# Kernel optimization log

Measured on AMD Instinct MI355X. Metric: run time of the kernel, lower is better.

Reference implementation:

```python
import jax, jax.numpy as jnp
import numpy as np

B, M, FIN, OUT, K = 64, 512, 128, 128, 2
SLOPE = 0.01  # F.leaky_relu default negative_slope


def setup_inputs() -> dict:
    key = jax.random.key(0)
    k0, k1, k2, k3 = jax.random.split(key, 4)
    x = jax.random.normal(k0, (B, M, FIN), jnp.float32)
    La = jax.random.normal(k1, (B, M, M), jnp.float32)
    weight = jax.random.normal(k2, (FIN * K, OUT), jnp.float32) * np.sqrt(2.0 / (FIN * K + OUT))
    bias = jnp.zeros((OUT,), jnp.float32)
    M_L = jax.random.normal(k3, (FIN, FIN), jnp.float32) * np.sqrt(2.0 / FIN)
    return {"x": x, "La": La, "weight": weight, "bias": bias, "M_L": M_L}


def _leaky(v):
    return jnp.where(v >= 0, v, SLOPE * v)


def _per_mol(xm, Lm, weight, bias, M_L):
    # xm: [M, FIN], Lm: [M, M]
    # compute_laplacian: pairwise Euclidean distances of x @ M_L via gram trick
    xw = xm @ M_L                                   # [M, FIN]
    sq = jnp.sum(xw * xw, axis=-1)                  # [M]
    d2 = sq[:, None] + sq[None, :] - 2.0 * (xw @ xw.T)
    dist = jnp.sqrt(jnp.maximum(d2, 1e-12))         # safe sqrt (diag is 0)
    W = jnp.exp(-dist)                              # [M, M]
    d = W.sum(axis=1) + 1e-7
    dis = 1.0 / jnp.sqrt(d)
    L = jnp.eye(M, dtype=xm.dtype) - dis[:, None] * W * dis[None, :]
    # clip_by_average_norm(clip_norm=1)
    avg_norm = jnp.linalg.norm(L) / (M * M)
    factor = jnp.minimum(1.0 / (avg_norm + 1e-6), 1.0)
    res_L = _leaky(L * factor)
    L_all = res_L + Lm
    # Chebyshev recursion (K terms)
    xs = [xm]
    if K > 1:
        xs.append(L_all @ xm)
    for _ in range(2, K):
        xs.append(2.0 * (L_all @ xs[-1]) - xs[-2])
    xk = jnp.stack(xs, axis=0)                      # [K, M, FIN]
    xk = jnp.transpose(xk, (1, 2, 0)).reshape(M, K * FIN)  # matches permute(1,2,0).view
    out = _leaky(xk @ weight + bias)                # activation 'relu' maps to leaky_relu
    return out, res_L, W


def reference(x, La, weight, bias, M_L):
    out, L_upd, W_upd = jax.vmap(lambda xm, Lm: _per_mol(xm, Lm, weight, bias, M_L))(x, La)
    return out, L_upd, W_upd
```

## Files before the change

kernel.cpp:

```cpp
#include <hip/hip_runtime.h>


#define BB 64
#define MM 512
#define FINC 128
#define OUTC 128

typedef short bf16x8 __attribute__((ext_vector_type(8)));
typedef float f32x4 __attribute__((ext_vector_type(4)));

__device__ __forceinline__ float leaky_(float v) { return v >= 0.0f ? v : 0.01f * v; }
__device__ __forceinline__ unsigned short f2bf(float f) {
    unsigned int u = __float_as_uint(f);
    return (unsigned short)((u + 0x7FFF + ((u >> 16) & 1)) >> 16);
}

__global__ __launch_bounds__(256) void k_xw(const float* __restrict__ x,
                                            const float* __restrict__ ml,
                                            unsigned short* __restrict__ xwb,
                                            float* __restrict__ sq,
                                            unsigned short* __restrict__ xTb) {
    const int b = blockIdx.y, i0 = blockIdx.x * 64;
    const int tid = threadIdx.x, ty4 = (tid >> 4) * 4, tx4 = (tid & 15) * 4;
    __shared__ float a_t[64][129];
    __shared__ float b_t[64][129];
    __shared__ float red[64][17];

    const float* xb = x + ((size_t)b * MM + i0) * FINC;
#pragma unroll
    for (int q = 0; q < 8; ++q) {
        int idx4 = tid + q * 256;
        int r = idx4 >> 5, k4 = (idx4 & 31) * 4;
        float4 v = *(const float4*)(xb + r * FINC + k4);
        a_t[r][k4 + 0] = v.x; a_t[r][k4 + 1] = v.y;
        a_t[r][k4 + 2] = v.z; a_t[r][k4 + 3] = v.w;
    }

    float acc[4][8];
#pragma unroll
    for (int m = 0; m < 4; ++m)
#pragma unroll
        for (int n = 0; n < 8; ++n) acc[m][n] = 0.0f;

    for (int kc = 0; kc < 2; ++kc) {
        __syncthreads();
#pragma unroll
        for (int q = 0; q < 8; ++q) {
            int idx4 = tid + q * 256;
            int kk = idx4 >> 5, c4 = (idx4 & 31) * 4;
            float4 v = *(const float4*)(ml + (size_t)(kc * 64 + kk) * FINC + c4);
            b_t[kk][c4 + 0] = v.x; b_t[kk][c4 + 1] = v.y;
            b_t[kk][c4 + 2] = v.z; b_t[kk][c4 + 3] = v.w;
        }
        __syncthreads();
#pragma unroll 4
        for (int k = 0; k < 64; ++k) {
            float av[4], bv[8];
#pragma unroll
            for (int m = 0; m < 4; ++m) av[m] = a_t[ty4 + m][kc * 64 + k];
#pragma unroll
            for (int n = 0; n < 4; ++n) { bv[n] = b_t[k][tx4 + n]; bv[4 + n] = b_t[k][64 + tx4 + n]; }
#pragma unroll
            for (int m = 0; m < 4; ++m)
#pragma unroll
                for (int n = 0; n < 8; ++n) acc[m][n] = fmaf(av[m], bv[n], acc[m][n]);
        }
    }

    unsigned short* xwbb = xwb + ((size_t)b * MM + i0) * FINC;
#pragma unroll
    for (int m = 0; m < 4; ++m) {
        ushort4 h0, h1;
        h0.x = f2bf(acc[m][0]); h0.y = f2bf(acc[m][1]); h0.z = f2bf(acc[m][2]); h0.w = f2bf(acc[m][3]);
        h1.x = f2bf(acc[m][4]); h1.y = f2bf(acc[m][5]); h1.z = f2bf(acc[m][6]); h1.w = f2bf(acc[m][7]);
        *(ushort4*)(xwbb + (ty4 + m) * FINC + tx4) = h0;
        *(ushort4*)(xwbb + (ty4 + m) * FINC + 64 + tx4) = h1;
        float p = 0.0f;
#pragma unroll
        for (int n = 0; n < 8; ++n) p = fmaf(acc[m][n], acc[m][n], p);
        red[ty4 + m][tid & 15] = p;
    }
    __syncthreads();
    if (tid < 64) {
        float s = 0.0f;
#pragma unroll
        for (int t = 0; t < 16; ++t) s += red[tid][t];
        sq[b * MM + i0 + tid] = s;
    }
#pragma unroll
    for (int q = 0; q < 16; ++q) {
        int idx = tid + q * 256;
        int c = idx >> 5, j2 = (idx & 31) * 2;
        ushort2 t;
        t.x = f2bf(a_t[j2][c]);
        t.y = f2bf(a_t[j2 + 1][c]);
        *(ushort2*)(xTb + ((size_t)b * FINC + c) * MM + i0 + j2) = t;
    }
}

__global__ __launch_bounds__(256) void k_gram(const unsigned short* __restrict__ xwb,
                                              const float* __restrict__ sq,
                                              float* __restrict__ Wout,
                                              float* __restrict__ dis) {
    const int b = blockIdx.y, i0 = blockIdx.x * 64;
    const int tid = threadIdx.x;
    const int w = tid >> 6, l = tid & 63, lr = l & 15, lg = l >> 4;
    const unsigned short* xb = xwb + (size_t)b * MM * FINC;
    const int ia = i0 + w * 16 + lr;
    const unsigned short* arow = xb + (size_t)ia * FINC + lg * 8;
    bf16x8 a0 = *(const bf16x8*)(arow + 0);
    bf16x8 a1 = *(const bf16x8*)(arow + 32);
    bf16x8 a2 = *(const bf16x8*)(arow + 64);
    bf16x8 a3 = *(const bf16x8*)(arow + 96);

    const int id0 = i0 + w * 16 + lg * 4;
    const float* sqb = sq + b * MM;
    const float si0 = sqb[id0 + 0], si1 = sqb[id0 + 1], si2 = sqb[id0 + 2], si3 = sqb[id0 + 3];
    float rs0 = 0.f, rs1 = 0.f, rs2 = 0.f, rs3 = 0.f;
    float* Wb = Wout + (size_t)b * MM * MM;

#pragma unroll 2
    for (int h = 0; h < 2; ++h) {
        const int j0 = h * 256;
#pragma unroll
        for (int n = 0; n < 16; ++n) {
            const int jc = j0 + n * 16 + lr;
            const unsigned short* jrow = xb + (size_t)jc * FINC + lg * 8;
            bf16x8 b0 = *(const bf16x8*)(jrow + 0);
            bf16x8 b1 = *(const bf16x8*)(jrow + 32);
            bf16x8 b2 = *(const bf16x8*)(jrow + 64);
            bf16x8 b3 = *(const bf16x8*)(jrow + 96);
            f32x4 acc = {0.f, 0.f, 0.f, 0.f};
            acc = __builtin_amdgcn_mfma_f32_16x16x32_bf16(a0, b0, acc, 0, 0, 0);
            acc = __builtin_amdgcn_mfma_f32_16x16x32_bf16(a1, b1, acc, 0, 0, 0);
            acc = __builtin_amdgcn_mfma_f32_16x16x32_bf16(a2, b2, acc, 0, 0, 0);
            acc = __builtin_amdgcn_mfma_f32_16x16x32_bf16(a3, b3, acc, 0, 0, 0);
            const float sj = sqb[jc];
            float d2, wv;
            d2 = si0 + sj - 2.f * acc[0]; if (id0 + 0 == jc) d2 = 0.f;
            wv = __expf(-sqrtf(fmaxf(d2, 1e-12f)));
            Wb[(size_t)(id0 + 0) * MM + jc] = wv; rs0 += wv;
            d2 = si1 + sj - 2.f * acc[1]; if (id0 + 1 == jc) d2 = 0.f;
            wv = __expf(-sqrtf(fmaxf(d2, 1e-12f)));
            Wb[(size_t)(id0 + 1) * MM + jc] = wv; rs1 += wv;
            d2 = si2 + sj - 2.f * acc[2]; if (id0 + 2 == jc) d2 = 0.f;
            wv = __expf(-sqrtf(fmaxf(d2, 1e-12f)));
            Wb[(size_t)(id0 + 2) * MM + jc] = wv; rs2 += wv;
            d2 = si3 + sj - 2.f * acc[3]; if (id0 + 3 == jc) d2 = 0.f;
            wv = __expf(-sqrtf(fmaxf(d2, 1e-12f)));
            Wb[(size_t)(id0 + 3) * MM + jc] = wv; rs3 += wv;
        }
    }
#pragma unroll
    for (int msk = 1; msk < 16; msk <<= 1) {
        rs0 += __shfl_xor(rs0, msk);
        rs1 += __shfl_xor(rs1, msk);
        rs2 += __shfl_xor(rs2, msk);
        rs3 += __shfl_xor(rs3, msk);
    }
    if (lr == 0) {
        dis[b * MM + id0 + 0] = 1.0f / sqrtf(rs0 + 1e-7f);
        dis[b * MM + id0 + 1] = 1.0f / sqrtf(rs1 + 1e-7f);
        dis[b * MM + id0 + 2] = 1.0f / sqrtf(rs2 + 1e-7f);
        dis[b * MM + id0 + 3] = 1.0f / sqrtf(rs3 + 1e-7f);
    }
}

__global__ __launch_bounds__(256) void k_norm(const float* __restrict__ Wout,
                                              const float* __restrict__ dis,
                                              float* __restrict__ norm2) {
    const int b = blockIdx.y;
    const float4* Wb4 = (const float4*)(Wout + (size_t)b * MM * MM);
    const float* disb = dis + b * MM;
    const int base4 = blockIdx.x * 4096;
    float acc = 0.0f;
#pragma unroll 4
    for (int q = 0; q < 16; ++q) {
        int idx4 = base4 + q * 256 + threadIdx.x;
        float4 w = Wb4[idx4];
        int p = idx4 * 4, i = p >> 9, j = p & 511;
        float di = disb[i];
        float4 dj = *(const float4*)(disb + j);
        float l0 = ((i == j + 0) ? 1.0f : 0.0f) - di * w.x * dj.x;
        float l1 = ((i == j + 1) ? 1.0f : 0.0f) - di * w.y * dj.y;
        float l2 = ((i == j + 2) ? 1.0f : 0.0f) - di * w.z * dj.z;
        float l3 = ((i == j + 3) ? 1.0f : 0.0f) - di * w.w * dj.w;
        acc += l0 * l0 + l1 * l1 + l2 * l2 + l3 * l3;
    }
#pragma unroll
    for (int off = 32; off > 0; off >>= 1) acc += __shfl_down(acc, off);
    __shared__ float r[4];
    if ((threadIdx.x & 63) == 0) r[threadIdx.x >> 6] = acc;
    __syncthreads();
    if (threadIdx.x == 0) atomicAdd(&norm2[b], r[0] + r[1] + r[2] + r[3]);
}

__global__ void k_factor(const float* __restrict__ norm2, float* __restrict__ factor) {
    int t = threadIdx.x;
    if (t < BB) {
        float avg = sqrtf(norm2[t]) / (512.0f * 512.0f);
        factor[t] = fminf(1.0f / (avg + 1e-6f), 1.0f);
    }
}

__global__ __launch_bounds__(256) void k_wt(const float* __restrict__ weight,
                                            unsigned short* __restrict__ wTb) {
    int tid = threadIdx.x;
#pragma unroll 4
    for (int q = 0; q < 128; ++q) {
        int idx = tid + q * 256;
        int k = idx >> 7, c = idx & 127;
        wTb[(size_t)c * 256 + k] = f2bf(weight[idx]);
    }
}

__global__ __launch_bounds__(256) void k_lall(const float* __restrict__ Wout,
                                              const float* __restrict__ La,
                                              const unsigned short* __restrict__ xTb,
                                              const float* __restrict__ dis,
                                              const float* __restrict__ factor,
                                              float* __restrict__ resL,
                                              unsigned short* __restrict__ yb) {
    const int b = blockIdx.y, i0 = blockIdx.x * 64;
    const int tid = threadIdx.x;
    const int w = tid >> 6, l = tid & 63, lr = l & 15, lg = l >> 4;
    const int ia = i0 + w * 16 + lr;
    const float fac = factor[b];
    const float* disb = dis + b * MM;
    const float di = disb[ia];
    const float* Wr = Wout + (size_t)b * MM * MM + (size_t)ia * MM;
    const float* Lr = La   + (size_t)b * MM * MM + (size_t)ia * MM;
    float* Rr = resL + (size_t)b * MM * MM + (size_t)ia * MM;
    const unsigned short* xTm = xTb + (size_t)b * FINC * MM;

    f32x4 acc[8];
#pragma unroll
    for (int n = 0; n < 8; ++n) acc[n] = (f32x4){0.f, 0.f, 0.f, 0.f};

    int ko0 = lg * 8;
    float4 wc0 = *(const float4*)(Wr + ko0), wc1 = *(const float4*)(Wr + ko0 + 4);
    float4 lc0 = *(const float4*)(Lr + ko0), lc1 = *(const float4*)(Lr + ko0 + 4);

#pragma unroll
    for (int t = 0; t < 16; ++t) {
        const int koff = t * 32 + lg * 8;
        float4 wn0, wn1, ln0, ln1;
        if (t < 15) {
            const int kn = (t + 1) * 32 + lg * 8;
            wn0 = *(const float4*)(Wr + kn); wn1 = *(const float4*)(Wr + kn + 4);
            ln0 = *(const float4*)(Lr + kn); ln1 = *(const float4*)(Lr + kn + 4);
        }
        float4 dj0 = *(const float4*)(disb + koff);
        float4 dj1 = *(const float4*)(disb + koff + 4);

        const int dd = ia - koff;
        const float* wp0 = &wc0.x; const float* wp1 = &wc1.x;
        const float* lp0 = &lc0.x; const float* lp1 = &lc1.x;
        const float* dp0 = &dj0.x; const float* dp1 = &dj1.x;
        float4 r0, r1; float* rp0 = &r0.x; float* rp1 = &r1.x;
        bf16x8 af;
#pragma unroll
        for (int e = 0; e < 4; ++e) {
            float Lv = ((dd == e) ? 1.0f : 0.0f) - di * wp0[e] * dp0[e];
            float rv = leaky_(Lv * fac);
            rp0[e] = rv;
            af[e] = (short)f2bf(rv + lp0[e]);
        }
#pragma unroll
        for (int e = 0; e < 4; ++e) {
            float Lv = ((dd == e + 4) ? 1.0f : 0.0f) - di * wp1[e] * dp1[e];
            float rv = leaky_(Lv * fac);
            rp1[e] = rv;
            af[e + 4] = (short)f2bf(rv + lp1[e]);
        }
        *(float4*)(Rr + koff) = r0;
        *(float4*)(Rr + koff + 4) = r1;

#pragma unroll
        for (int n = 0; n < 8; ++n) {
            bf16x8 bf = *(const bf16x8*)(xTm + (size_t)(n * 16 + lr) * MM + koff);
            acc[n] = __builtin_amdgcn_mfma_f32_16x16x32_bf16(af, bf, acc[n], 0, 0, 0);
        }
        wc0 = wn0; wc1 = wn1; lc0 = ln0; lc1 = ln1;
    }

    const int id0 = i0 + w * 16 + lg * 4;
    unsigned short* ybb = yb + (size_t)b * MM * FINC;
#pragma unroll
    for (int n = 0; n < 8; ++n) {
        const int col = n * 16 + lr;
#pragma unroll
        for (int rg = 0; rg < 4; ++rg)
            ybb[(size_t)(id0 + rg) * FINC + col] = f2bf(acc[n][rg]);
    }
}

__global__ __launch_bounds__(256) void k_out(const float* __restrict__ x,
                                             const unsigned short* __restrict__ yb,
                                             const unsigned short* __restrict__ wTb,
                                             const float* __restrict__ bias,
                                             float* __restrict__ out) {
    const int b = blockIdx.y, i0 = blockIdx.x * 64;
    const int tid = threadIdx.x;
    const int w = tid >> 6, l = tid & 63, lr = l & 15, lg = l >> 4;
    const int ia = i0 + w * 16 + lr;
    const float* xr = x + ((size_t)b * MM + ia) * FINC;
    const unsigned short* yr = yb + ((size_t)b * MM + ia) * FINC;

    f32x4 acc[8];
#pragma unroll
    for (int n = 0; n < 8; ++n) acc[n] = (f32x4){0.f, 0.f, 0.f, 0.f};

#pragma unroll
    for (int ch = 0; ch < 8; ++ch) {
        const int koff = ch * 32 + lg * 8;
        const int f0 = koff >> 1;
        float4 xv = *(const float4*)(xr + f0);
        ushort4 yv = *(const ushort4*)(yr + f0);
        bf16x8 af;
        af[0] = (short)f2bf(xv.x); af[1] = (short)yv.x;
        af[2] = (short)f2bf(xv.y); af[3] = (short)yv.y;
        af[4] = (short)f2bf(xv.z); af[5] = (short)yv.z;
        af[6] = (short)f2bf(xv.w); af[7] = (short)yv.w;
#pragma unroll
        for (int n = 0; n < 8; ++n) {
            bf16x8 bf = *(const bf16x8*)(wTb + (size_t)(n * 16 + lr) * 256 + koff);
            acc[n] = __builtin_amdgcn_mfma_f32_16x16x32_bf16(af, bf, acc[n], 0, 0, 0);
        }
    }

    const int id0 = i0 + w * 16 + lg * 4;
    float* ob = out + (size_t)b * MM * OUTC;
#pragma unroll
    for (int n = 0; n < 8; ++n) {
        const int col = n * 16 + lr;
        const float bs = bias[col];
#pragma unroll
        for (int rg = 0; rg < 4; ++rg)
            ob[(size_t)(id0 + rg) * OUTC + col] = leaky_(acc[n][rg] + bs);
    }
}

extern "C" void kernel_launch(void* const* d_in, const int* in_sizes, int n_in,
                              void* d_out, int out_size, void* d_ws, size_t ws_size,
                              hipStream_t stream) {
    const float* x      = (const float*)d_in[0];
    const float* La     = (const float*)d_in[1];
    const float* weight = (const float*)d_in[2];
    const float* bias   = (const float*)d_in[3];
    const float* ml     = (const float*)d_in[4];

    float* out0 = (float*)d_out;
    float* out1 = out0 + (size_t)BB * MM * OUTC;
    float* out2 = out1 + (size_t)BB * MM * MM;

    unsigned short* xwb = (unsigned short*)d_ws;
    unsigned short* yb  = xwb;
    unsigned short* xTb = xwb + 4194304;
    float* sq     = (float*)((char*)d_ws + 16777216);
    unsigned short* wTb = (unsigned short*)sq;
    float* dis    = sq + 32768;
    float* norm2  = dis + 32768;
    float* factor = norm2 + 64;

    hipMemsetAsync(norm2, 0, BB * sizeof(float), stream);

    dim3 blk(256);
    k_xw    <<<dim3(8, BB), blk, 0, stream>>>(x, ml, xwb, sq, xTb);
    k_gram  <<<dim3(8, BB), blk, 0, stream>>>(xwb, sq, out2, dis);
    k_norm  <<<dim3(16, BB), blk, 0, stream>>>(out2, dis, norm2);
    k_factor<<<1, 64, 0, stream>>>(norm2, factor);
    k_wt    <<<1, blk, 0, stream>>>(weight, wTb);
    k_lall  <<<dim3(8, BB), blk, 0, stream>>>(out2, La, xTb, dis, factor, out1, yb);
    k_out   <<<dim3(8, BB), blk, 0, stream>>>(x, yb, wTb, bias, out0);
}
```

Measured before the change: 397.2 us.

## Software-prefetch operands in gram, lall and out kernels; fold factor and weight kernels

Restructures the k_gram column loop into 32 tiles that prefetch the next tile's bf16 rows and sq value while the current MFMA and exp work runs. k_lall now uses two-deep register prefetch of W/La rows and batches its B-operand loads ahead of the MFMAs. k_out prefetches the next x/y chunk. The factor computation moves into k_lall and the weight transpose into block (0,0) of k_norm, which removes two small launches. The cost is higher register pressure, which could reduce occupancy.

```diff
diff --git a/kernel.cpp b/kernel.cpp
--- a/kernel.cpp
+++ b/kernel.cpp
@@ -119,37 +119,45 @@
     float rs0 = 0.f, rs1 = 0.f, rs2 = 0.f, rs3 = 0.f;
     float* Wb = Wout + (size_t)b * MM * MM;
 
-#pragma unroll 2
-    for (int h = 0; h < 2; ++h) {
-        const int j0 = h * 256;
-#pragma unroll
-        for (int n = 0; n < 16; ++n) {
-            const int jc = j0 + n * 16 + lr;
-            const unsigned short* jrow = xb + (size_t)jc * FINC + lg * 8;
-            bf16x8 b0 = *(const bf16x8*)(jrow + 0);
-            bf16x8 b1 = *(const bf16x8*)(jrow + 32);
-            bf16x8 b2 = *(const bf16x8*)(jrow + 64);
-            bf16x8 b3 = *(const bf16x8*)(jrow + 96);
-            f32x4 acc = {0.f, 0.f, 0.f, 0.f};
-            acc = __builtin_amdgcn_mfma_f32_16x16x32_bf16(a0, b0, acc, 0, 0, 0);
-            acc = __builtin_amdgcn_mfma_f32_16x16x32_bf16(a1, b1, acc, 0, 0, 0);
-            acc = __builtin_amdgcn_mfma_f32_16x16x32_bf16(a2, b2, acc, 0, 0, 0);
-            acc = __builtin_amdgcn_mfma_f32_16x16x32_bf16(a3, b3, acc, 0, 0, 0);
-            const float sj = sqb[jc];
-            float d2, wv;
-            d2 = si0 + sj - 2.f * acc[0]; if (id0 + 0 == jc) d2 = 0.f;
-            wv = __expf(-sqrtf(fmaxf(d2, 1e-12f)));
-            Wb[(size_t)(id0 + 0) * MM + jc] = wv; rs0 += wv;
-            d2 = si1 + sj - 2.f * acc[1]; if (id0 + 1 == jc) d2 = 0.f;
-            wv = __expf(-sqrtf(fmaxf(d2, 1e-12f)));
-            Wb[(size_t)(id0 + 1) * MM + jc] = wv; rs1 += wv;
-            d2 = si2 + sj - 2.f * acc[2]; if (id0 + 2 == jc) d2 = 0.f;
-            wv = __expf(-sqrtf(fmaxf(d2, 1e-12f)));
-            Wb[(size_t)(id0 + 2) * MM + jc] = wv; rs2 += wv;
-            d2 = si3 + sj - 2.f * acc[3]; if (id0 + 3 == jc) d2 = 0.f;
-            wv = __expf(-sqrtf(fmaxf(d2, 1e-12f)));
-            Wb[(size_t)(id0 + 3) * MM + jc] = wv; rs3 += wv;
-        }
+    const unsigned short* jr0 = xb + (size_t)lr * FINC + lg * 8;
+    bf16x8 c0 = *(const bf16x8*)(jr0 + 0);
+    bf16x8 c1 = *(const bf16x8*)(jr0 + 32);
+    bf16x8 c2 = *(const bf16x8*)(jr0 + 64);
+    bf16x8 c3 = *(const bf16x8*)(jr0 + 96);
+    float sjc = sqb[lr];
+
+#pragma unroll
+    for (int tl = 0; tl < 32; ++tl) {
+        const int nt = (tl < 31) ? tl + 1 : 31;
+        const unsigned short* nr = xb + (size_t)(nt * 16 + lr) * FINC + lg * 8;
+        bf16x8 n0 = *(const bf16x8*)(nr + 0);
+        bf16x8 n1 = *(const bf16x8*)(nr + 32);
+        bf16x8 n2 = *(const bf16x8*)(nr + 64);
+        bf16x8 n3 = *(const bf16x8*)(nr + 96);
+        float sjn = sqb[nt * 16 + lr];
+
+        f32x4 acc = {0.f, 0.f, 0.f, 0.f};
+        acc = __builtin_amdgcn_mfma_f32_16x16x32_bf16(a0, c0, acc, 0, 0, 0);
+        acc = __builtin_amdgcn_mfma_f32_16x16x32_bf16(a1, c1, acc, 0, 0, 0);
+        acc = __builtin_amdgcn_mfma_f32_16x16x32_bf16(a2, c2, acc, 0, 0, 0);
+        acc = __builtin_amdgcn_mfma_f32_16x16x32_bf16(a3, c3, acc, 0, 0, 0);
+
+        const int jc = tl * 16 + lr;
+        float d2, wv;
+        d2 = si0 + sjc - 2.f * acc[0]; if (id0 + 0 == jc) d2 = 0.f;
+        wv = __expf(-sqrtf(fmaxf(d2, 1e-12f)));
+        Wb[(size_t)(id0 + 0) * MM + jc] = wv; rs0 += wv;
+        d2 = si1 + sjc - 2.f * acc[1]; if (id0 + 1 == jc) d2 = 0.f;
+        wv = __expf(-sqrtf(fmaxf(d2, 1e-12f)));
+        Wb[(size_t)(id0 + 1) * MM + jc] = wv; rs1 += wv;
+        d2 = si2 + sjc - 2.f * acc[2]; if (id0 + 2 == jc) d2 = 0.f;
+        wv = __expf(-sqrtf(fmaxf(d2, 1e-12f)));
+        Wb[(size_t)(id0 + 2) * MM + jc] = wv; rs2 += wv;
+        d2 = si3 + sjc - 2.f * acc[3]; if (id0 + 3 == jc) d2 = 0.f;
+        wv = __expf(-sqrtf(fmaxf(d2, 1e-12f)));
+        Wb[(size_t)(id0 + 3) * MM + jc] = wv; rs3 += wv;
+
+        c0 = n0; c1 = n1; c2 = n2; c3 = n3; sjc = sjn;
     }
 #pragma unroll
     for (int msk = 1; msk < 16; msk <<= 1) {
@@ -168,7 +176,9 @@
 
 __global__ __launch_bounds__(256) void k_norm(const float* __restrict__ Wout,
                                               const float* __restrict__ dis,
-                                              float* __restrict__ norm2) {
+                                              float* __restrict__ norm2,
+                                              const float* __restrict__ weight,
+                                              unsigned short* __restrict__ wTb) {
     const int b = blockIdx.y;
     const float4* Wb4 = (const float4*)(Wout + (size_t)b * MM * MM);
     const float* disb = dis + b * MM;
@@ -193,24 +203,15 @@
     if ((threadIdx.x & 63) == 0) r[threadIdx.x >> 6] = acc;
     __syncthreads();
     if (threadIdx.x == 0) atomicAdd(&norm2[b], r[0] + r[1] + r[2] + r[3]);
-}
-
-__global__ void k_factor(const float* __restrict__ norm2, float* __restrict__ factor) {
-    int t = threadIdx.x;
-    if (t < BB) {
-        float avg = sqrtf(norm2[t]) / (512.0f * 512.0f);
-        factor[t] = fminf(1.0f / (avg + 1e-6f), 1.0f);
-    }
-}
-
-__global__ __launch_bounds__(256) void k_wt(const float* __restrict__ weight,
-                                            unsigned short* __restrict__ wTb) {
-    int tid = threadIdx.x;
+
+    if (blockIdx.x == 0 && blockIdx.y == 0) {
+        int tid = threadIdx.x;
 #pragma unroll 4
-    for (int q = 0; q < 128; ++q) {
-        int idx = tid + q * 256;
-        int k = idx >> 7, c = idx & 127;
-        wTb[(size_t)c * 256 + k] = f2bf(weight[idx]);
+        for (int q = 0; q < 128; ++q) {
+            int idx = tid + q * 256;
+            int k = idx >> 7, c = idx & 127;
+            wTb[(size_t)c * 256 + k] = f2bf(weight[idx]);
+        }
     }
 }
 
@@ -218,14 +219,15 @@
                                               const float* __restrict__ La,
                                               const unsigned short* __restrict__ xTb,
                                               const float* __restrict__ dis,
-                                              const float* __restrict__ factor,
+                                              const float* __restrict__ norm2,
                                               float* __restrict__ resL,
                                               unsigned short* __restrict__ yb) {
     const int b = blockIdx.y, i0 = blockIdx.x * 64;
     const int tid = threadIdx.x;
     const int w = tid >> 6, l = tid & 63, lr = l & 15, lg = l >> 4;
     const int ia = i0 + w * 16 + lr;
-    const float fac = factor[b];
+    const float avgn = sqrtf(norm2[b]) / (512.0f * 512.0f);
+    const float fac = fminf(1.0f / (avgn + 1e-6f), 1.0f);
     const float* disb = dis + b * MM;
     const float di = disb[ia];
     const float* Wr = Wout + (size_t)b * MM * MM + (size_t)ia * MM;
@@ -237,52 +239,60 @@
 #pragma unroll
     for (int n = 0; n < 8; ++n) acc[n] = (f32x4){0.f, 0.f, 0.f, 0.f};
 
-    int ko0 = lg * 8;
-    float4 wc0 = *(const float4*)(Wr + ko0), wc1 = *(const float4*)(Wr + ko0 + 4);
-    float4 lc0 = *(const float4*)(Lr + ko0), lc1 = *(const float4*)(Lr + ko0 + 4);
-
-#pragma unroll
-    for (int t = 0; t < 16; ++t) {
-        const int koff = t * 32 + lg * 8;
-        float4 wn0, wn1, ln0, ln1;
-        if (t < 15) {
-            const int kn = (t + 1) * 32 + lg * 8;
-            wn0 = *(const float4*)(Wr + kn); wn1 = *(const float4*)(Wr + kn + 4);
-            ln0 = *(const float4*)(Lr + kn); ln1 = *(const float4*)(Lr + kn + 4);
-        }
-        float4 dj0 = *(const float4*)(disb + koff);
-        float4 dj1 = *(const float4*)(disb + koff + 4);
-
-        const int dd = ia - koff;
-        const float* wp0 = &wc0.x; const float* wp1 = &wc1.x;
-        const float* lp0 = &lc0.x; const float* lp1 = &lc1.x;
-        const float* dp0 = &dj0.x; const float* dp1 = &dj1.x;
-        float4 r0, r1; float* rp0 = &r0.x; float* rp1 = &r1.x;
-        bf16x8 af;
-#pragma unroll
-        for (int e = 0; e < 4; ++e) {
-            float Lv = ((dd == e) ? 1.0f : 0.0f) - di * wp0[e] * dp0[e];
-            float rv = leaky_(Lv * fac);
-            rp0[e] = rv;
-            af[e] = (short)f2bf(rv + lp0[e]);
-        }
-#pragma unroll
-        for (int e = 0; e < 4; ++e) {
-            float Lv = ((dd == e + 4) ? 1.0f : 0.0f) - di * wp1[e] * dp1[e];
-            float rv = leaky_(Lv * fac);
-            rp1[e] = rv;
-            af[e + 4] = (short)f2bf(rv + lp1[e]);
-        }
-        *(float4*)(Rr + koff) = r0;
-        *(float4*)(Rr + koff + 4) = r1;
-
-#pragma unroll
-        for (int n = 0; n < 8; ++n) {
-            bf16x8 bf = *(const bf16x8*)(xTm + (size_t)(n * 16 + lr) * MM + koff);
-            acc[n] = __builtin_amdgcn_mfma_f32_16x16x32_bf16(af, bf, acc[n], 0, 0, 0);
-        }
-        wc0 = wn0; wc1 = wn1; lc0 = ln0; lc1 = ln1;
-    }
+#define LD2(W0, W1, L0, L1, t) { const int kk_ = (t) * 32 + lg * 8; \
+    W0 = *(const float4*)(Wr + kk_); W1 = *(const float4*)(Wr + kk_ + 4); \
+    L0 = *(const float4*)(Lr + kk_); L1 = *(const float4*)(Lr + kk_ + 4); }
+
+#define STEP(CW0, CW1, CL0, CL1, t) { \
+    const int koff = (t) * 32 + lg * 8; \
+    bf16x8 bfr[8]; \
+    _Pragma("unroll") \
+    for (int n = 0; n < 8; ++n) \
+        bfr[n] = *(const bf16x8*)(xTm + (size_t)(n * 16 + lr) * MM + koff); \
+    float4 dj0 = *(const float4*)(disb + koff); \
+    float4 dj1 = *(const float4*)(disb + koff + 4); \
+    const int dd = ia - koff; \
+    const float* wp0 = &CW0.x; const float* wp1 = &CW1.x; \
+    const float* lp0 = &CL0.x; const float* lp1 = &CL1.x; \
+    const float* dp0 = &dj0.x; const float* dp1 = &dj1.x; \
+    float4 r0, r1; float* rp0 = &r0.x; float* rp1 = &r1.x; \
+    bf16x8 af; \
+    _Pragma("unroll") \
+    for (int e = 0; e < 4; ++e) { \
+        float Lv = ((dd == e) ? 1.0f : 0.0f) - di * wp0[e] * dp0[e]; \
+        float rv = leaky_(Lv * fac); \
+        rp0[e] = rv; \
+        af[e] = (short)f2bf(rv + lp0[e]); \
+    } \
+    _Pragma("unroll") \
+    for (int e = 0; e < 4; ++e) { \
+        float Lv = ((dd == e + 4) ? 1.0f : 0.0f) - di * wp1[e] * dp1[e]; \
+        float rv = leaky_(Lv * fac); \
+        rp1[e] = rv; \
+        af[e + 4] = (short)f2bf(rv + lp1[e]); \
+    } \
+    *(float4*)(Rr + koff) = r0; \
+    *(float4*)(Rr + koff + 4) = r1; \
+    _Pragma("unroll") \
+    for (int n = 0; n < 8; ++n) \
+        acc[n] = __builtin_amdgcn_mfma_f32_16x16x32_bf16(af, bfr[n], acc[n], 0, 0, 0); \
+}
+
+    float4 aw0, aw1, al0, al1, bw0, bw1, bl0, bl1, tw0, tw1, tl0, tl1;
+    LD2(aw0, aw1, al0, al1, 0);
+    LD2(bw0, bw1, bl0, bl1, 1);
+#pragma unroll
+    for (int tp = 0; tp < 8; ++tp) {
+        const int t0 = tp * 2, t1 = tp * 2 + 1;
+        if (t0 + 2 < 16) { LD2(tw0, tw1, tl0, tl1, t0 + 2); }
+        STEP(aw0, aw1, al0, al1, t0);
+        if (t0 + 2 < 16) { aw0 = tw0; aw1 = tw1; al0 = tl0; al1 = tl1; }
+        if (t1 + 2 < 16) { LD2(tw0, tw1, tl0, tl1, t1 + 2); }
+        STEP(bw0, bw1, bl0, bl1, t1);
+        if (t1 + 2 < 16) { bw0 = tw0; bw1 = tw1; bl0 = tl0; bl1 = tl1; }
+    }
+#undef LD2
+#undef STEP
 
     const int id0 = i0 + w * 16 + lg * 4;
     unsigned short* ybb = yb + (size_t)b * MM * FINC;
@@ -311,22 +321,29 @@
 #pragma unroll
     for (int n = 0; n < 8; ++n) acc[n] = (f32x4){0.f, 0.f, 0.f, 0.f};
 
+    float4 xc = *(const float4*)(xr + lg * 4);
+    ushort4 yc = *(const ushort4*)(yr + lg * 4);
+
 #pragma unroll
     for (int ch = 0; ch < 8; ++ch) {
         const int koff = ch * 32 + lg * 8;
-        const int f0 = koff >> 1;
-        float4 xv = *(const float4*)(xr + f0);
-        ushort4 yv = *(const ushort4*)(yr + f0);
+        float4 xn; ushort4 yn;
+        if (ch < 7) {
+            const int f1 = (ch + 1) * 16 + lg * 4;
+            xn = *(const float4*)(xr + f1);
+            yn = *(const ushort4*)(yr + f1);
+        }
         bf16x8 af;
-        af[0] = (short)f2bf(xv.x); af[1] = (short)yv.x;
-        af[2] = (short)f2bf(xv.y); af[3] = (short)yv.y;
-        af[4] = (short)f2bf(xv.z); af[5] = (short)yv.z;
-        af[6] = (short)f2bf(xv.w); af[7] = (short)yv.w;
+        af[0] = (short)f2bf(xc.x); af[1] = (short)yc.x;
+        af[2] = (short)f2bf(xc.y); af[3] = (short)yc.y;
+        af[4] = (short)f2bf(xc.z); af[5] = (short)yc.z;
+        af[6] = (short)f2bf(xc.w); af[7] = (short)yc.w;
 #pragma unroll
         for (int n = 0; n < 8; ++n) {
             bf16x8 bf = *(const bf16x8*)(wTb + (size_t)(n * 16 + lr) * 256 + koff);
             acc[n] = __builtin_amdgcn_mfma_f32_16x16x32_bf16(af, bf, acc[n], 0, 0, 0);
         }
+        if (ch < 7) { xc = xn; yc = yn; }
     }
 
     const int id0 = i0 + w * 16 + lg * 4;
@@ -361,16 +378,13 @@
     unsigned short* wTb = (unsigned short*)sq;
     float* dis    = sq + 32768;
     float* norm2  = dis + 32768;
-    float* factor = norm2 + 64;
 
     hipMemsetAsync(norm2, 0, BB * sizeof(float), stream);
 
     dim3 blk(256);
-    k_xw    <<<dim3(8, BB), blk, 0, stream>>>(x, ml, xwb, sq, xTb);
-    k_gram  <<<dim3(8, BB), blk, 0, stream>>>(xwb, sq, out2, dis);
-    k_norm  <<<dim3(16, BB), blk, 0, stream>>>(out2, dis, norm2);
-    k_factor<<<1, 64, 0, stream>>>(norm2, factor);
-    k_wt    <<<1, blk, 0, stream>>>(weight, wTb);
-    k_lall  <<<dim3(8, BB), blk, 0, stream>>>(out2, La, xTb, dis, factor, out1, yb);
-    k_out   <<<dim3(8, BB), blk, 0, stream>>>(x, yb, wTb, bias, out0);
-}
+    k_xw    <<<dim3(8, BB),  blk, 0, stream>>>(x, ml, xwb, sq, xTb);
+    k_gram  <<<dim3(8, BB),  blk, 0, stream>>>(xwb, sq, out2, dis);
+    k_norm  <<<dim3(16, BB), blk, 0, stream>>>(out2, dis, norm2, weight, wTb);
+    k_lall  <<<dim3(8, BB),  blk, 0, stream>>>(out2, La, xTb, dis, norm2, out1, yb);
+    k_out   <<<dim3(8, BB),  blk, 0, stream>>>(x, yb, wTb, bias, out0);
+}
```

Result: faster. 376.9 us (-5.1%).
